# Kernel optimization log

Hardware: AMD Instinct MI355X
Metric: run time of the kernel (lower is better)

The kernel has to match this reference:

```python
import jax, jax.numpy as jnp
import numpy as np

LN_EPS = 1e-5

def setup_inputs() -> dict:
    num_nodes, embed_dim, bs, E = 10000, 64, 32, 200000
    key = jax.random.key(0)
    ks = jax.random.split(key, 8)
    d_in = 2 * embed_dim + 1  # msg_dim = 1
    d_h = 4 * embed_dim
    return {
        "users": jax.random.randint(ks[0], (E,), 0, num_nodes * bs),
        "items": jax.random.randint(ks[1], (E,), 0, num_nodes * bs),
        "messages": jax.random.normal(ks[2], (E,), dtype=jnp.float32),
        "bs": bs,
        "user_emb": jax.random.normal(ks[3], (num_nodes, embed_dim), dtype=jnp.float32) * 0.02,
        "item_emb": jax.random.normal(ks[4], (num_nodes, embed_dim), dtype=jnp.float32) * 0.02,
        "W1": jax.random.normal(ks[5], (d_in, d_h), dtype=jnp.float32) * 0.02,
        "b1": jnp.zeros((d_h,), dtype=jnp.float32),
        "ln_g": jnp.ones((d_h,), dtype=jnp.float32),
        "ln_b": jnp.zeros((d_h,), dtype=jnp.float32),
        "W2": jax.random.normal(ks[6], (d_h, d_h), dtype=jnp.float32) * 0.02,
        "b2": jnp.zeros((d_h,), dtype=jnp.float32),
    }

def reference(users, items, messages, bs, user_emb, item_emb, W1, b1, ln_g, ln_b, W2, b2):
    num_nodes, embed_dim = user_emb.shape
    N = num_nodes * bs
    msgs = messages.astype(jnp.float32).reshape(-1, 1)          # [E,1]
    ue = user_emb[users % num_nodes]                             # [E,D]
    ie = item_emb[items % num_nodes]                             # [E,D]
    x = jnp.concatenate([ue, ie, msgs], axis=-1)                 # [E,2D+1]
    h = x @ W1 + b1                                              # [E,4D]
    mu = jnp.mean(h, axis=-1, keepdims=True)
    var = jnp.mean(jnp.square(h - mu), axis=-1, keepdims=True)
    hn = (h - mu) * jax.lax.rsqrt(var + LN_EPS) * ln_g + ln_b
    enc = hn @ W2 + b2                                           # [E,4D]
    uu, iu, ug, ig = jnp.split(enc, 4, axis=-1)                  # each [E,D]
    user_state = jnp.zeros((N, embed_dim), jnp.float32).at[users].add(uu)
    item_state = jnp.zeros((N, embed_dim), jnp.float32).at[items].add(iu)
    user_global = jnp.zeros((N, embed_dim), jnp.float32).at[users].add(ug)
    item_global = jnp.zeros((N, embed_dim), jnp.float32).at[items].add(ig)
    # reshape (num_nodes, bs, D) -> (bs, num_nodes, D)
    up = jnp.transpose(user_global.reshape(num_nodes, bs, embed_dim), (1, 0, 2))
    ip = jnp.transpose(item_global.reshape(num_nodes, bs, embed_dim), (1, 0, 2))
    up = jnp.mean(up, axis=1, keepdims=True)                     # [bs,1,D]
    ip = jnp.mean(ip, axis=1, keepdims=True)
    ret_u = jnp.transpose(user_state.reshape(num_nodes, bs, embed_dim), (1, 0, 2)) + up
    ret_i = jnp.transpose(item_state.reshape(num_nodes, bs, embed_dim), (1, 0, 2)) + ip
    return (ret_u, ret_i)
```

## Files before the change

kernel.cpp:

```cpp
#include <hip/hip_runtime.h>
#include <hip/hip_bf16.h>


typedef __attribute__((ext_vector_type(8))) short bf8_t;
typedef __attribute__((ext_vector_type(4))) float f32x4;

union FragU { bf8_t f; unsigned int u[4]; };

static __device__ __forceinline__ unsigned short f2bf(float f) {
    unsigned int x = __float_as_uint(f);
    return (unsigned short)((x + 0x7fffu + ((x >> 16) & 1u)) >> 16);
}
#define B2F_LO(u) __uint_as_float((u) << 16)
#define B2F_HI(u) __uint_as_float((u) & 0xffff0000u)

__global__ void zero_f4_kernel(float4* p, int n4) {
    int i = blockIdx.x * 256 + threadIdx.x;
    int stride = gridDim.x * 256;
    float4 z = make_float4(0.f, 0.f, 0.f, 0.f);
    for (; i < n4; i += stride) p[i] = z;
}

__global__ void convert_kernel(const float* __restrict__ W1, const float* __restrict__ W2,
                               const float* __restrict__ uemb, const float* __restrict__ iemb,
                               unsigned short* __restrict__ w1f, unsigned short* __restrict__ w2f,
                               unsigned short* __restrict__ uembb, unsigned short* __restrict__ iembb,
                               int nemb4) {
    int idx = blockIdx.x * 256 + threadIdx.x;
    if (idx < 4096) {
        int l = idx & 63, fr = idx >> 6;
        int ks = fr & 3, nt = fr >> 2;
        int n = nt * 16 + (l & 15), g = l >> 4;
        unsigned short v[8];
#pragma unroll
        for (int e = 0; e < 8; e++) {
            int k = ks * 32 + ((e < 4) ? (4 * g + e) : (16 + 4 * g + (e - 4)));
            v[e] = f2bf(W1[k * 256 + n]);
        }
        uint4 pk;
        pk.x = (unsigned)v[0] | ((unsigned)v[1] << 16);
        pk.y = (unsigned)v[2] | ((unsigned)v[3] << 16);
        pk.z = (unsigned)v[4] | ((unsigned)v[5] << 16);
        pk.w = (unsigned)v[6] | ((unsigned)v[7] << 16);
        *(uint4*)&w1f[idx * 8] = pk;
    } else if (idx < 12288) {
        int t = idx - 4096;
        int l = t & 63, fr = t >> 6;
        int ks = fr & 7, nt = fr >> 3;
        int n = nt * 16 + (l & 15), g = l >> 4;
        unsigned short v[8];
#pragma unroll
        for (int e = 0; e < 8; e++) {
            int k = ks * 32 + ((e < 4) ? (4 * g + e) : (16 + 4 * g + (e - 4)));
            v[e] = f2bf(W2[k * 256 + n]);
        }
        uint4 pk;
        pk.x = (unsigned)v[0] | ((unsigned)v[1] << 16);
        pk.y = (unsigned)v[2] | ((unsigned)v[3] << 16);
        pk.z = (unsigned)v[4] | ((unsigned)v[5] << 16);
        pk.w = (unsigned)v[6] | ((unsigned)v[7] << 16);
        *(uint4*)&w2f[t * 8] = pk;
    }
    if (nemb4 > 0) {
        int total = gridDim.x * 256;
        for (int i = idx; i < 2 * nemb4; i += total) {
            int isU = (i < nemb4);
            int j = isU ? i : i - nemb4;
            float4 v = isU ? ((const float4*)uemb)[j] : ((const float4*)iemb)[j];
            ushort4 p;
            p.x = f2bf(v.x); p.y = f2bf(v.y); p.z = f2bf(v.z); p.w = f2bf(v.w);
            unsigned short* dst = isU ? uembb : iembb;
            *(ushort4*)&dst[(long)j * 4] = p;
        }
    }
}

__global__ __launch_bounds__(512, 2)
void encode_mfma_kernel(const int* __restrict__ users, const int* __restrict__ items,
                        const float* __restrict__ msgs,
                        const float* __restrict__ uemb, const float* __restrict__ iemb,
                        const unsigned short* __restrict__ uembb, const unsigned short* __restrict__ iembb,
                        const float* __restrict__ W1, const float* __restrict__ b1,
                        const float* __restrict__ ln_g, const float* __restrict__ ln_b,
                        const float* __restrict__ b2,
                        const unsigned short* __restrict__ w1f, const unsigned short* __restrict__ w2f,
                        float* __restrict__ out, float* __restrict__ glob,
                        int E, int num_nodes, int bs, long out_half, int usebf) {
    __shared__ __align__(16) unsigned short xhb[64 * 256];
    __shared__ __align__(16) float gacc[4096];
    __shared__ __align__(16) float msgs_s[64];
    __shared__ __align__(16) int ubase_s[64], ibase_s[64];

    const int tid = threadIdx.x;
    const int w = tid >> 6;
    const int l = tid & 63;
    const int g = l >> 4;
    const int m16 = l & 15;
    const int nnD = num_nodes * 64;

    for (int i = tid; i < 4096; i += 512) gacc[i] = 0.f;

    bf8_t w1frag[2][4], w2frag[2][8];
#pragma unroll
    for (int ntl = 0; ntl < 2; ntl++) {
        int nt = w * 2 + ntl;
#pragma unroll
        for (int ks = 0; ks < 4; ks++)
            w1frag[ntl][ks] = *(const bf8_t*)&w1f[((nt * 4 + ks) * 64 + l) * 8];
#pragma unroll
        for (int ks = 0; ks < 8; ks++)
            w2frag[ntl][ks] = *(const bf8_t*)&w2f[((nt * 8 + ks) * 64 + l) * 8];
    }

    float b1v[2], w128v[2], b2v[2];
#pragma unroll
    for (int ntl = 0; ntl < 2; ntl++) {
        int j = w * 32 + ntl * 16 + m16;
        b1v[ntl] = b1[j];
        w128v[ntl] = W1[128 * 256 + j];
        b2v[ntl] = b2[j];
    }
    float* outi = out + out_half;

    const int nTiles = (E + 63) >> 6;
    for (int tile = blockIdx.x; tile < nTiles; tile += gridDim.x) {
        const int e0 = tile << 6;
        __syncthreads();

        if (tid < 64) {
            int ev = e0 + tid;
            if (ev < E) {
                int u = users[ev], it = items[ev];
                int ub = u % bs, un = u / bs, ib = it % bs, in_ = it / bs;
                ubase_s[tid] = (ub * nnD + un * 64) | (ub << 26);
                ibase_s[tid] = (ib * nnD + in_ * 64) | (ib << 26);
                msgs_s[tid] = msgs[ev];
            } else {
                ubase_s[tid] = -1; ibase_s[tid] = -1; msgs_s[tid] = 0.f;
            }
        }
        for (int idx = tid; idx < 1024; idx += 512) {
            int e = idx >> 4, q = idx & 15;
            int ev = e0 + e;
            uint4 v = make_uint4(0u, 0u, 0u, 0u);
            if (ev < E) {
                if (usebf) {
                    if (q < 8) { int u = users[ev] % num_nodes; v = *(const uint4*)&uembb[(long)u * 64 + q * 8]; }
                    else       { int it = items[ev] % num_nodes; v = *(const uint4*)&iembb[(long)it * 64 + (q - 8) * 8]; }
                } else {
                    const float* src; long base;
                    if (q < 8) { int u = users[ev] % num_nodes; src = uemb; base = (long)u * 64 + q * 8; }
                    else       { int it = items[ev] % num_nodes; src = iemb; base = (long)it * 64 + (q - 8) * 8; }
                    float4 a0 = *(const float4*)&src[base];
                    float4 a1 = *(const float4*)&src[base + 4];
                    v.x = (unsigned)f2bf(a0.x) | ((unsigned)f2bf(a0.y) << 16);
                    v.y = (unsigned)f2bf(a0.z) | ((unsigned)f2bf(a0.w) << 16);
                    v.z = (unsigned)f2bf(a1.x) | ((unsigned)f2bf(a1.y) << 16);
                    v.w = (unsigned)f2bf(a1.z) | ((unsigned)f2bf(a1.w) << 16);
                }
            }
            int byte = (q * 16) ^ ((e & 7) << 4);
            *(uint4*)&xhb[e * 128 + (byte >> 1)] = v;
        }
        __syncthreads();

        f32x4 acc[4][2];
#pragma unroll
        for (int mt = 0; mt < 4; mt++) {
            const float* mgp = &msgs_s[mt * 16 + 4 * g];
            float mg[4] = {mgp[0], mgp[1], mgp[2], mgp[3]};
#pragma unroll
            for (int ntl = 0; ntl < 2; ntl++) {
                f32x4 a;
#pragma unroll
                for (int r = 0; r < 4; r++) a[r] = fmaf(mg[r], w128v[ntl], b1v[ntl]);
                acc[mt][ntl] = a;
            }
        }
#pragma unroll
        for (int ks = 0; ks < 4; ks++) {
            FragU a[4];
#pragma unroll
            for (int mt = 0; mt < 4; mt++) {
                int i = mt * 16 + m16;
                int bir0 = (ks * 64 + 8 * g) ^ ((i & 7) << 4);
                int bir1 = (ks * 64 + 32 + 8 * g) ^ ((i & 7) << 4);
                uint2 c0 = *(const uint2*)&xhb[i * 128 + (bir0 >> 1)];
                uint2 c1 = *(const uint2*)&xhb[i * 128 + (bir1 >> 1)];
                a[mt].u[0] = c0.x; a[mt].u[1] = c0.y; a[mt].u[2] = c1.x; a[mt].u[3] = c1.y;
            }
#pragma unroll
            for (int ntl = 0; ntl < 2; ntl++)
#pragma unroll
                for (int mt = 0; mt < 4; mt++)
                    acc[mt][ntl] = __builtin_amdgcn_mfma_f32_16x16x32_bf16(
                        a[mt].f, w1frag[ntl][ks], acc[mt][ntl], 0, 0, 0);
        }
        __syncthreads();

#pragma unroll
        for (int mt = 0; mt < 4; mt++)
#pragma unroll
            for (int ntl = 0; ntl < 2; ntl++)
#pragma unroll
                for (int r = 0; r < 4; r++) {
                    int e = mt * 16 + 4 * g + r;
                    int j = w * 32 + ntl * 16 + m16;
                    int byte = (2 * j) ^ ((e & 15) << 4);
                    xhb[e * 256 + (byte >> 1)] = f2bf(acc[mt][ntl][r]);
                }
        __syncthreads();

#pragma unroll
        for (int it = 0; it < 4; it++) {
            int e = w * 8 + it * 2 + (l >> 5);
            int slot = l & 31;
            int byte = (slot * 16) ^ ((e & 15) << 4);
            uint4 hv = *(const uint4*)&xhb[e * 256 + (byte >> 1)];
            float f0 = B2F_LO(hv.x), f1 = B2F_HI(hv.x);
            float f2 = B2F_LO(hv.y), f3 = B2F_HI(hv.y);
            float f4 = B2F_LO(hv.z), f5 = B2F_HI(hv.z);
            float f6 = B2F_LO(hv.w), f7 = B2F_HI(hv.w);
            float s1 = ((f0 + f1) + (f2 + f3)) + ((f4 + f5) + (f6 + f7));
            float s2 = ((f0*f0 + f1*f1) + (f2*f2 + f3*f3)) + ((f4*f4 + f5*f5) + (f6*f6 + f7*f7));
#pragma unroll
            for (int mk = 1; mk <= 16; mk <<= 1) {
                s1 += __shfl_xor(s1, mk);
                s2 += __shfl_xor(s2, mk);
            }
            float mu = s1 * (1.f / 256.f);
            float var = s2 * (1.f / 256.f) - mu * mu;
            float rs = rsqrtf(var + 1e-5f);
            int jb = (slot ^ (e & 15)) * 8;
            float4 g0 = *(const float4*)&ln_g[jb];
            float4 g1 = *(const float4*)&ln_g[jb + 4];
            float4 bb0 = *(const float4*)&ln_b[jb];
            float4 bb1 = *(const float4*)&ln_b[jb + 4];
            float n0 = fmaf((f0 - mu) * rs, g0.x, bb0.x);
            float n1 = fmaf((f1 - mu) * rs, g0.y, bb0.y);
            float n2 = fmaf((f2 - mu) * rs, g0.z, bb0.z);
            float n3 = fmaf((f3 - mu) * rs, g0.w, bb0.w);
            float n4 = fmaf((f4 - mu) * rs, g1.x, bb1.x);
            float n5 = fmaf((f5 - mu) * rs, g1.y, bb1.y);
            float n6 = fmaf((f6 - mu) * rs, g1.z, bb1.z);
            float n7 = fmaf((f7 - mu) * rs, g1.w, bb1.w);
            uint4 pv;
            pv.x = (unsigned)f2bf(n0) | ((unsigned)f2bf(n1) << 16);
            pv.y = (unsigned)f2bf(n2) | ((unsigned)f2bf(n3) << 16);
            pv.z = (unsigned)f2bf(n4) | ((unsigned)f2bf(n5) << 16);
            pv.w = (unsigned)f2bf(n6) | ((unsigned)f2bf(n7) << 16);
            *(uint4*)&xhb[e * 256 + (byte >> 1)] = pv;
        }
        __syncthreads();

#pragma unroll
        for (int mt = 0; mt < 4; mt++)
#pragma unroll
            for (int ntl = 0; ntl < 2; ntl++) {
                f32x4 a;
#pragma unroll
                for (int r = 0; r < 4; r++) a[r] = b2v[ntl];
                acc[mt][ntl] = a;
            }
#pragma unroll
        for (int ks = 0; ks < 8; ks++) {
            FragU a[4];
#pragma unroll
            for (int mt = 0; mt < 4; mt++) {
                int i = mt * 16 + m16;
                int bir0 = (ks * 64 + 8 * g) ^ ((i & 15) << 4);
                int bir1 = (ks * 64 + 32 + 8 * g) ^ ((i & 15) << 4);
                uint2 c0 = *(const uint2*)&xhb[i * 256 + (bir0 >> 1)];
                uint2 c1 = *(const uint2*)&xhb[i * 256 + (bir1 >> 1)];
                a[mt].u[0] = c0.x; a[mt].u[1] = c0.y; a[mt].u[2] = c1.x; a[mt].u[3] = c1.y;
            }
#pragma unroll
            for (int ntl = 0; ntl < 2; ntl++)
#pragma unroll
                for (int mt = 0; mt < 4; mt++)
                    acc[mt][ntl] = __builtin_amdgcn_mfma_f32_16x16x32_bf16(
                        a[mt].f, w2frag[ntl][ks], acc[mt][ntl], 0, 0, 0);
        }

        const int q = w >> 1;
        const int dbase = (w & 1) * 32;
        const int* barr = (q & 1) ? ibase_s : ubase_s;
#pragma unroll
        for (int mt = 0; mt < 4; mt++) {
            int4 bb = *(const int4*)&barr[mt * 16 + 4 * g];
            int bvv[4] = {bb.x, bb.y, bb.z, bb.w};
#pragma unroll
            for (int ntl = 0; ntl < 2; ntl++) {
                int d = dbase + ntl * 16 + m16;
#pragma unroll
                for (int r = 0; r < 4; r++) {
                    int v = bvv[r];
                    if (v >= 0) {
                        float val = acc[mt][ntl][r];
                        if (q == 0)      atomicAdd(&out[(v & 0x03FFFFFF) + d], val);
                        else if (q == 1) atomicAdd(&outi[(v & 0x03FFFFFF) + d], val);
                        else if (q == 2) atomicAdd(&gacc[(v >> 26) * 64 + d], val);
                        else             atomicAdd(&gacc[2048 + (v >> 26) * 64 + d], val);
                    }
                }
            }
        }
    }

    __syncthreads();
    for (int i = tid; i < 4096; i += 512) {
        float v = gacc[i];
        if (v != 0.f) atomicAdd(&glob[i], v);
    }
}

__global__ void finalize_kernel(float* __restrict__ out, const float* __restrict__ glob,
                                long out_half, long nnD, float inv_nodes, int n4) {
    int i4 = blockIdx.x * 256 + threadIdx.x;
    int stride = gridDim.x * 256;
    for (; i4 < n4; i4 += stride) {
        long i = (long)i4 * 4;
        int half = (i >= out_half) ? 1 : 0;
        long r = half ? (i - out_half) : i;
        int b = (int)(r / nnD);
        int dq = (int)(i & 63);
        float4 gv = *(const float4*)&glob[half * 2048 + b * 64 + dq];
        float4 o = ((float4*)out)[i4];
        o.x += gv.x * inv_nodes;
        o.y += gv.y * inv_nodes;
        o.z += gv.z * inv_nodes;
        o.w += gv.w * inv_nodes;
        ((float4*)out)[i4] = o;
    }
}

extern "C" void kernel_launch(void* const* d_in, const int* in_sizes, int n_in,
                              void* d_out, int out_size, void* d_ws, size_t ws_size,
                              hipStream_t stream) {
    const int* users = (const int*)d_in[0];
    const int* items = (const int*)d_in[1];
    const float* msgs = (const float*)d_in[2];
    const float* uemb = (const float*)d_in[4];
    const float* iemb = (const float*)d_in[5];
    const float* W1 = (const float*)d_in[6];
    const float* b1 = (const float*)d_in[7];
    const float* ln_g = (const float*)d_in[8];
    const float* ln_b = (const float*)d_in[9];
    const float* W2 = (const float*)d_in[10];
    const float* b2 = (const float*)d_in[11];

    const int E = in_sizes[0];
    const int dh = in_sizes[7];
    const int D = dh / 4;
    const int num_nodes = in_sizes[4] / D;
    const long out_half = (long)out_size / 2;
    const int bs = (int)(out_half / ((long)num_nodes * D));

    float* out = (float*)d_out;
    float* glob = (float*)d_ws;
    unsigned short* w1f = (unsigned short*)((char*)d_ws + 16384);
    unsigned short* w2f = (unsigned short*)((char*)d_ws + 16384 + 65536);
    size_t embb_off = 16384 + 65536 + 131072;
    size_t embb_bytes = (size_t)num_nodes * 64 * 2;
    int usebf = (ws_size >= embb_off + 2 * embb_bytes) ? 1 : 0;
    unsigned short* uembb = usebf ? (unsigned short*)((char*)d_ws + embb_off) : nullptr;
    unsigned short* iembb = usebf ? (unsigned short*)((char*)d_ws + embb_off + embb_bytes) : nullptr;
    int nemb4 = usebf ? (num_nodes * 16) : 0;

    zero_f4_kernel<<<2048, 256, 0, stream>>>((float4*)out, out_size / 4);
    zero_f4_kernel<<<4, 256, 0, stream>>>((float4*)glob, 4096 / 4);
    convert_kernel<<<256, 256, 0, stream>>>(W1, W2, uemb, iemb, w1f, w2f, uembb, iembb, nemb4);

    encode_mfma_kernel<<<512, 512, 0, stream>>>(
        users, items, msgs, uemb, iemb, uembb, iembb,
        W1, b1, ln_g, ln_b, b2, w1f, w2f, out, glob,
        E, num_nodes, bs, out_half, usebf);

    finalize_kernel<<<2048, 256, 0, stream>>>(out, glob, out_half,
                                              (long)num_nodes * 64, 1.0f / num_nodes,
                                              out_size / 4);
}
```

Before: 479.7 us.

## Use 1024-thread blocks with one N-tile per wave in encode kernel

Restructures the fused encode kernel so each block has 16 waves, and each wave owns one 16-column N-tile instead of two. This halves the per-wave weight fragments and accumulators, cutting register pressure so more waves can be resident. The grid shrinks to 256 blocks of 1024 threads, so each block processes more edge tiles and the shared-memory histogram flush runs fewer times. Trade-offs: each wave now re-reads the A fragments from LDS for less MFMA work, and the larger blocks pay more for barriers. The zero-fill kernel is also switched to long indexing.

```diff
diff --git a/kernel.cpp b/kernel.cpp
--- a/kernel.cpp
+++ b/kernel.cpp
@@ -14,9 +14,9 @@
 #define B2F_LO(u) __uint_as_float((u) << 16)
 #define B2F_HI(u) __uint_as_float((u) & 0xffff0000u)
 
-__global__ void zero_f4_kernel(float4* p, int n4) {
-    int i = blockIdx.x * 256 + threadIdx.x;
-    int stride = gridDim.x * 256;
+__global__ void zero_f4_kernel(float4* p, long n4) {
+    long i = (long)blockIdx.x * 256 + threadIdx.x;
+    long stride = (long)gridDim.x * 256;
     float4 z = make_float4(0.f, 0.f, 0.f, 0.f);
     for (; i < n4; i += stride) p[i] = z;
 }
@@ -75,7 +75,7 @@
     }
 }
 
-__global__ __launch_bounds__(512, 2)
+__global__ __launch_bounds__(1024, 4)
 void encode_mfma_kernel(const int* __restrict__ users, const int* __restrict__ items,
                         const float* __restrict__ msgs,
                         const float* __restrict__ uemb, const float* __restrict__ iemb,
@@ -98,28 +98,20 @@
     const int m16 = l & 15;
     const int nnD = num_nodes * 64;
 
-    for (int i = tid; i < 4096; i += 512) gacc[i] = 0.f;
-
-    bf8_t w1frag[2][4], w2frag[2][8];
-#pragma unroll
-    for (int ntl = 0; ntl < 2; ntl++) {
-        int nt = w * 2 + ntl;
-#pragma unroll
-        for (int ks = 0; ks < 4; ks++)
-            w1frag[ntl][ks] = *(const bf8_t*)&w1f[((nt * 4 + ks) * 64 + l) * 8];
-#pragma unroll
-        for (int ks = 0; ks < 8; ks++)
-            w2frag[ntl][ks] = *(const bf8_t*)&w2f[((nt * 8 + ks) * 64 + l) * 8];
-    }
-
-    float b1v[2], w128v[2], b2v[2];
-#pragma unroll
-    for (int ntl = 0; ntl < 2; ntl++) {
-        int j = w * 32 + ntl * 16 + m16;
-        b1v[ntl] = b1[j];
-        w128v[ntl] = W1[128 * 256 + j];
-        b2v[ntl] = b2[j];
-    }
+    for (int i = tid; i < 4096; i += 1024) gacc[i] = 0.f;
+
+    bf8_t w1frag[4], w2frag[8];
+#pragma unroll
+    for (int ks = 0; ks < 4; ks++)
+        w1frag[ks] = *(const bf8_t*)&w1f[((w * 4 + ks) * 64 + l) * 8];
+#pragma unroll
+    for (int ks = 0; ks < 8; ks++)
+        w2frag[ks] = *(const bf8_t*)&w2f[((w * 8 + ks) * 64 + l) * 8];
+
+    const int j = w * 16 + m16;
+    const float b1v = b1[j];
+    const float w128v = W1[128 * 256 + j];
+    const float b2v = b2[j];
     float* outi = out + out_half;
 
     const int nTiles = (E + 63) >> 6;
@@ -139,8 +131,8 @@
                 ubase_s[tid] = -1; ibase_s[tid] = -1; msgs_s[tid] = 0.f;
             }
         }
-        for (int idx = tid; idx < 1024; idx += 512) {
-            int e = idx >> 4, q = idx & 15;
+        {
+            int e = tid >> 4, q = tid & 15;
             int ev = e0 + e;
             uint4 v = make_uint4(0u, 0u, 0u, 0u);
             if (ev < E) {
@@ -164,18 +156,14 @@
         }
         __syncthreads();
 
-        f32x4 acc[4][2];
+        f32x4 acc[4];
 #pragma unroll
         for (int mt = 0; mt < 4; mt++) {
             const float* mgp = &msgs_s[mt * 16 + 4 * g];
-            float mg[4] = {mgp[0], mgp[1], mgp[2], mgp[3]};
-#pragma unroll
-            for (int ntl = 0; ntl < 2; ntl++) {
-                f32x4 a;
-#pragma unroll
-                for (int r = 0; r < 4; r++) a[r] = fmaf(mg[r], w128v[ntl], b1v[ntl]);
-                acc[mt][ntl] = a;
-            }
+            f32x4 a;
+#pragma unroll
+            for (int r = 0; r < 4; r++) a[r] = fmaf(mgp[r], w128v, b1v);
+            acc[mt] = a;
         }
 #pragma unroll
         for (int ks = 0; ks < 4; ks++) {
@@ -190,30 +178,25 @@
                 a[mt].u[0] = c0.x; a[mt].u[1] = c0.y; a[mt].u[2] = c1.x; a[mt].u[3] = c1.y;
             }
 #pragma unroll
-            for (int ntl = 0; ntl < 2; ntl++)
-#pragma unroll
-                for (int mt = 0; mt < 4; mt++)
-                    acc[mt][ntl] = __builtin_amdgcn_mfma_f32_16x16x32_bf16(
-                        a[mt].f, w1frag[ntl][ks], acc[mt][ntl], 0, 0, 0);
+            for (int mt = 0; mt < 4; mt++)
+                acc[mt] = __builtin_amdgcn_mfma_f32_16x16x32_bf16(
+                    a[mt].f, w1frag[ks], acc[mt], 0, 0, 0);
         }
         __syncthreads();
 
 #pragma unroll
         for (int mt = 0; mt < 4; mt++)
 #pragma unroll
-            for (int ntl = 0; ntl < 2; ntl++)
-#pragma unroll
-                for (int r = 0; r < 4; r++) {
-                    int e = mt * 16 + 4 * g + r;
-                    int j = w * 32 + ntl * 16 + m16;
-                    int byte = (2 * j) ^ ((e & 15) << 4);
-                    xhb[e * 256 + (byte >> 1)] = f2bf(acc[mt][ntl][r]);
-                }
-        __syncthreads();
-
-#pragma unroll
-        for (int it = 0; it < 4; it++) {
-            int e = w * 8 + it * 2 + (l >> 5);
+            for (int r = 0; r < 4; r++) {
+                int e = mt * 16 + 4 * g + r;
+                int byte = (2 * j) ^ ((e & 15) << 4);
+                xhb[e * 256 + (byte >> 1)] = f2bf(acc[mt][r]);
+            }
+        __syncthreads();
+
+#pragma unroll
+        for (int it = 0; it < 2; it++) {
+            int e = w * 4 + it * 2 + (l >> 5);
             int slot = l & 31;
             int byte = (slot * 16) ^ ((e & 15) << 4);
             uint4 hv = *(const uint4*)&xhb[e * 256 + (byte >> 1)];
@@ -254,14 +237,12 @@
         __syncthreads();
 
 #pragma unroll
-        for (int mt = 0; mt < 4; mt++)
-#pragma unroll
-            for (int ntl = 0; ntl < 2; ntl++) {
-                f32x4 a;
-#pragma unroll
-                for (int r = 0; r < 4; r++) a[r] = b2v[ntl];
-                acc[mt][ntl] = a;
-            }
+        for (int mt = 0; mt < 4; mt++) {
+            f32x4 a;
+#pragma unroll
+            for (int r = 0; r < 4; r++) a[r] = b2v;
+            acc[mt] = a;
+        }
 #pragma unroll
         for (int ks = 0; ks < 8; ks++) {
             FragU a[4];
@@ -275,40 +256,34 @@
                 a[mt].u[0] = c0.x; a[mt].u[1] = c0.y; a[mt].u[2] = c1.x; a[mt].u[3] = c1.y;
             }
 #pragma unroll
-            for (int ntl = 0; ntl < 2; ntl++)
-#pragma unroll
-                for (int mt = 0; mt < 4; mt++)
-                    acc[mt][ntl] = __builtin_amdgcn_mfma_f32_16x16x32_bf16(
-                        a[mt].f, w2frag[ntl][ks], acc[mt][ntl], 0, 0, 0);
-        }
-
-        const int q = w >> 1;
-        const int dbase = (w & 1) * 32;
+            for (int mt = 0; mt < 4; mt++)
+                acc[mt] = __builtin_amdgcn_mfma_f32_16x16x32_bf16(
+                    a[mt].f, w2frag[ks], acc[mt], 0, 0, 0);
+        }
+
+        const int q = w >> 2;
+        const int d = (w & 3) * 16 + m16;
         const int* barr = (q & 1) ? ibase_s : ubase_s;
 #pragma unroll
         for (int mt = 0; mt < 4; mt++) {
             int4 bb = *(const int4*)&barr[mt * 16 + 4 * g];
             int bvv[4] = {bb.x, bb.y, bb.z, bb.w};
 #pragma unroll
-            for (int ntl = 0; ntl < 2; ntl++) {
-                int d = dbase + ntl * 16 + m16;
-#pragma unroll
-                for (int r = 0; r < 4; r++) {
-                    int v = bvv[r];
-                    if (v >= 0) {
-                        float val = acc[mt][ntl][r];
-                        if (q == 0)      atomicAdd(&out[(v & 0x03FFFFFF) + d], val);
-                        else if (q == 1) atomicAdd(&outi[(v & 0x03FFFFFF) + d], val);
-                        else if (q == 2) atomicAdd(&gacc[(v >> 26) * 64 + d], val);
-                        else             atomicAdd(&gacc[2048 + (v >> 26) * 64 + d], val);
-                    }
+            for (int r = 0; r < 4; r++) {
+                int v = bvv[r];
+                if (v >= 0) {
+                    float val = acc[mt][r];
+                    if (q == 0)      atomicAdd(&out[(v & 0x03FFFFFF) + d], val);
+                    else if (q == 1) atomicAdd(&outi[(v & 0x03FFFFFF) + d], val);
+                    else if (q == 2) atomicAdd(&gacc[(v >> 26) * 64 + d], val);
+                    else             atomicAdd(&gacc[2048 + (v >> 26) * 64 + d], val);
                 }
             }
         }
     }
 
     __syncthreads();
-    for (int i = tid; i < 4096; i += 512) {
+    for (int i = tid; i < 4096; i += 1024) {
         float v = gacc[i];
         if (v != 0.f) atomicAdd(&glob[i], v);
     }
@@ -359,19 +334,19 @@
     float* out = (float*)d_out;
     float* glob = (float*)d_ws;
     unsigned short* w1f = (unsigned short*)((char*)d_ws + 16384);
-    unsigned short* w2f = (unsigned short*)((char*)d_ws + 16384 + 65536);
-    size_t embb_off = 16384 + 65536 + 131072;
+    unsigned short* w2f = (unsigned short*)((char*)d_ws + 81920);
+    size_t embb_off = 212992;
     size_t embb_bytes = (size_t)num_nodes * 64 * 2;
     int usebf = (ws_size >= embb_off + 2 * embb_bytes) ? 1 : 0;
     unsigned short* uembb = usebf ? (unsigned short*)((char*)d_ws + embb_off) : nullptr;
     unsigned short* iembb = usebf ? (unsigned short*)((char*)d_ws + embb_off + embb_bytes) : nullptr;
     int nemb4 = usebf ? (num_nodes * 16) : 0;
 
-    zero_f4_kernel<<<2048, 256, 0, stream>>>((float4*)out, out_size / 4);
+    zero_f4_kernel<<<2048, 256, 0, stream>>>((float4*)out, (long)out_size / 4);
     zero_f4_kernel<<<4, 256, 0, stream>>>((float4*)glob, 4096 / 4);
     convert_kernel<<<256, 256, 0, stream>>>(W1, W2, uemb, iemb, w1f, w2f, uembb, iembb, nemb4);
 
-    encode_mfma_kernel<<<512, 512, 0, stream>>>(
+    encode_mfma_kernel<<<256, 1024, 0, stream>>>(
         users, items, msgs, uemb, iemb, uembb, iembb,
         W1, b1, ln_g, ln_b, b2, w1f, w2f, out, glob,
         E, num_nodes, bs, out_half, usebf);
```

New measurement: 506.5 us. 1.06x slower.
